# Kernel tuning notes

Hardware: AMD Instinct MI355X
Metric: run time of the kernel (lower is better)

Reference implementation:

```python
import jax, jax.numpy as jnp
import numpy as np

OUT_SIZE = 7
SAMPLE_NUM = 2
FINEST_SCALE = 56.0
STRIDES = (4, 8, 16, 32)
IMG_H, IMG_W = 800.0, 1216.0


def roi_align(feat, rois, out_size, spatial_scale, sr):
    """Vectorized RoIAlign (aligned=False / mmdet legacy semantics).
    feat: [B,C,H,W]; rois: [K,5] (batch_idx, x1, y1, x2, y2). Returns [K,C,out,out]."""
    B, C, H, W = feat.shape
    K = rois.shape[0]
    ft = jnp.transpose(feat, (0, 2, 3, 1))  # [B,H,W,C] for channel-last gathers
    b = rois[:, 0].astype(jnp.int32)
    x1 = rois[:, 1] * spatial_scale
    y1 = rois[:, 2] * spatial_scale
    x2 = rois[:, 3] * spatial_scale
    y2 = rois[:, 4] * spatial_scale
    roi_w = jnp.maximum(x2 - x1, 1.0)
    roi_h = jnp.maximum(y2 - y1, 1.0)
    bin_w = roi_w / out_size
    bin_h = roi_h / out_size
    G = out_size * sr  # sample grid points per spatial dim
    g = (jnp.arange(G, dtype=feat.dtype) + 0.5) / sr  # sub-bin centers in bin units
    ys = y1[:, None] + g[None, :] * bin_h[:, None]  # [K,G]
    xs = x1[:, None] + g[None, :] * bin_w[:, None]  # [K,G]
    # validity (points outside [-1, H]/[-1, W] contribute 0)
    vy = (ys >= -1.0) & (ys <= H)
    vx = (xs >= -1.0) & (xs <= W)
    valid = vy[:, :, None] & vx[:, None, :]  # [K,G,G]
    # clamp into the map, then bilinear interpolate
    ysc = jnp.clip(ys, 0.0, H - 1)
    xsc = jnp.clip(xs, 0.0, W - 1)
    y0 = jnp.floor(ysc)
    x0 = jnp.floor(xsc)
    ly = ysc - y0
    lx = xsc - x0
    y0i = y0.astype(jnp.int32)
    x0i = x0.astype(jnp.int32)

    def gather(yi, xi):  # yi:[K,G], xi:[K,G] -> [K,G,G,C]
        yc = jnp.clip(yi, 0, H - 1)
        xc = jnp.clip(xi, 0, W - 1)
        return ft[b[:, None, None], yc[:, :, None], xc[:, None, :], :]

    wy0 = (1.0 - ly)[:, :, None, None]
    wy1 = ly[:, :, None, None]
    wx0 = (1.0 - lx)[:, None, :, None]
    wx1 = lx[:, None, :, None]
    val = (gather(y0i, x0i) * (wy0 * wx0)
           + gather(y0i, x0i + 1) * (wy0 * wx1)
           + gather(y0i + 1, x0i) * (wy1 * wx0)
           + gather(y0i + 1, x0i + 1) * (wy1 * wx1))  # [K,G,G,C]
    val = val * valid[..., None]
    # average the sr x sr samples in each output bin
    val = val.reshape(K, out_size, sr, out_size, sr, C).mean(axis=(2, 4))
    return jnp.transpose(val, (0, 3, 1, 2))  # [K,C,out,out]


def map_roi_levels(rois, num_levels):
    scale = jnp.sqrt((rois[:, 3] - rois[:, 1] + 1.0) * (rois[:, 4] - rois[:, 2] + 1.0))
    lvl = jnp.floor(jnp.log2(scale / FINEST_SCALE + 1e-6))
    return jnp.clip(lvl, 0, num_levels - 1).astype(jnp.int32)


def setup_inputs() -> dict:
    key = jax.random.key(0)
    ks = jax.random.split(key, 10)
    feat0 = jax.random.normal(ks[0], (2, 256, 200, 304), dtype=jnp.float32)
    feat1 = jax.random.normal(ks[1], (2, 256, 100, 152), dtype=jnp.float32)
    feat2 = jax.random.normal(ks[2], (2, 256, 50, 76), dtype=jnp.float32)
    feat3 = jax.random.normal(ks[3], (2, 256, 25, 38), dtype=jnp.float32)
    K = 1024
    b = jax.random.randint(ks[4], (K,), 0, 2).astype(jnp.float32)
    # log-uniform box sizes in [16, 600] px so all 4 FPN levels are used
    logw = jax.random.uniform(ks[5], (K,), minval=np.log(16.0), maxval=np.log(600.0))
    logh = jax.random.uniform(ks[6], (K,), minval=np.log(16.0), maxval=np.log(600.0))
    w = jnp.exp(logw)
    h = jnp.exp(logh)
    cx = jax.random.uniform(ks[7], (K,), minval=0.0, maxval=IMG_W)
    cy = jax.random.uniform(ks[8], (K,), minval=0.0, maxval=IMG_H)
    x1 = jnp.clip(cx - w / 2, 0.0, IMG_W - 2.0)
    y1 = jnp.clip(cy - h / 2, 0.0, IMG_H - 2.0)
    x2 = jnp.clip(cx + w / 2, x1 + 1.0, IMG_W - 1.0)
    y2 = jnp.clip(cy + h / 2, y1 + 1.0, IMG_H - 1.0)
    rois = jnp.stack([b, x1, y1, x2, y2], axis=1).astype(jnp.float32)
    return {"feat0": feat0, "feat1": feat1, "feat2": feat2, "feat3": feat3, "rois": rois}


def reference(feat0, feat1, feat2, feat3, rois):
    feats = [feat0, feat1, feat2, feat3]
    num_levels = len(feats)
    lvls = map_roi_levels(rois, num_levels)  # [K]
    K = rois.shape[0]
    C = feats[0].shape[1]
    out = jnp.zeros((K, C, OUT_SIZE, OUT_SIZE), dtype=feats[0].dtype)
    for i in range(num_levels):
        pooled = roi_align(feats[i], rois, OUT_SIZE, 1.0 / STRIDES[i], SAMPLE_NUM)
        out = out + jnp.where((lvls == i)[:, None, None, None], pooled, 0.0)
    return out
```

## Files before the change

### kernel.cpp

```cpp
#include <hip/hip_runtime.h>
#include <math.h>


#define OUT_SZ 7
#define NCH 256
#define NBINS 49
#define NGROUPS 4

__global__ __launch_bounds__(256, 6)
void roi_align_direct(const float* __restrict__ f0, const float* __restrict__ f1,
                      const float* __restrict__ f2, const float* __restrict__ f3,
                      const float* __restrict__ rois,
                      float* __restrict__ out)
{
    const int k = blockIdx.x;
    const int g = blockIdx.y;
    const int t = threadIdx.x;
    const int w    = t >> 6;
    const int lane = t & 63;

    float rb   = rois[k * 5 + 0];
    float rix1 = rois[k * 5 + 1];
    float riy1 = rois[k * 5 + 2];
    float rix2 = rois[k * 5 + 3];
    float riy2 = rois[k * 5 + 4];

    float scale = sqrtf((rix2 - rix1 + 1.0f) * (riy2 - riy1 + 1.0f));
    int lvl = (int)floorf(log2f(scale * (1.0f / 56.0f) + 1e-6f));
    lvl = lvl < 0 ? 0 : (lvl > 3 ? 3 : lvl);

    float ss = 1.0f / (float)(4 << lvl);
    float x1 = rix1 * ss, y1 = riy1 * ss;
    float rw = fmaxf(rix2 * ss - x1, 1.0f);
    float rh = fmaxf(riy2 * ss - y1, 1.0f);
    float bw = rw * (1.0f / OUT_SZ);
    float bh = rh * (1.0f / OUT_SZ);
    const int H = 800  >> (2 + lvl);
    const int W = 1216 >> (2 + lvl);
    const float fH = (float)H, fW = (float)W;
    const float* fb = (lvl == 0) ? f0 : (lvl == 1) ? f1 : (lvl == 2) ? f2 : f3;
    const int HW = H * W;

    if (lane >= NBINS) return;
    const int bin = lane;
    const int oy = bin / OUT_SZ;
    const int ox = bin - oy * OUT_SZ;

    float lx[2], fvx[2]; int cx[2];
#pragma unroll
    for (int j = 0; j < 2; ++j) {
        float xs = x1 + ((float)(2 * ox + j) + 0.5f) * 0.5f * bw;
        fvx[j] = (xs >= -1.0f && xs <= fW) ? 1.0f : 0.0f;
        float xc = fminf(fmaxf(xs, 0.0f), fW - 1.0f);
        int x0 = (int)floorf(xc);
        x0 = min(x0, W - 2);
        lx[j] = xc - (float)x0;
        cx[j] = x0;
    }
    float ly[2], fvy[2]; int ry[2];
#pragma unroll
    for (int i = 0; i < 2; ++i) {
        float ysv = y1 + ((float)(2 * oy + i) + 0.5f) * 0.5f * bh;
        fvy[i] = (ysv >= -1.0f && ysv <= fH) ? 1.0f : 0.0f;
        float yc = fminf(fmaxf(ysv, 0.0f), fH - 1.0f);
        int y0 = (int)floorf(yc);
        y0 = min(y0, H - 2);
        ly[i] = yc - (float)y0;
        ry[i] = y0;
    }
    float wv00 = fvy[0] * fvx[0], wv01 = fvy[0] * fvx[1];
    float wv10 = fvy[1] * fvx[0], wv11 = fvy[1] * fvx[1];

    int off[8];
#pragma unroll
    for (int r = 0; r < 4; ++r) {
        int row = ry[r >> 1] + (r & 1);
        off[2 * r + 0] = row * W + cx[0];
        off[2 * r + 1] = row * W + cx[1];
    }

    const int ch0 = g * 64 + w;
    const float* chp = fb + (size_t)((int)rb * NCH + ch0) * HW;
    float* outp = out + ((size_t)k * NCH + ch0) * NBINS + bin;

#pragma unroll 2
    for (int i = 0; i < 16; ++i) {
        float v0[8], v1[8];
#pragma unroll
        for (int q = 0; q < 8; ++q) {
            v0[q] = chp[off[q]];
            v1[q] = chp[off[q] + 1];
        }
        float h[8];
#pragma unroll
        for (int q = 0; q < 8; ++q)
            h[q] = fmaf(lx[q & 1], v1[q] - v0[q], v0[q]);

        float s00 = fmaf(ly[0], h[2] - h[0], h[0]);
        float s01 = fmaf(ly[0], h[3] - h[1], h[1]);
        float s10 = fmaf(ly[1], h[6] - h[4], h[4]);
        float s11 = fmaf(ly[1], h[7] - h[5], h[5]);

        float acc = wv00 * s00 + wv01 * s01 + wv10 * s10 + wv11 * s11;
        *outp = acc * 0.25f;

        chp  += 4 * (size_t)HW;
        outp += 4 * NBINS;
    }
}

extern "C" void kernel_launch(void* const* d_in, const int* in_sizes, int n_in,
                              void* d_out, int out_size, void* d_ws, size_t ws_size,
                              hipStream_t stream)
{
    const float* f0   = (const float*)d_in[0];
    const float* f1   = (const float*)d_in[1];
    const float* f2   = (const float*)d_in[2];
    const float* f3   = (const float*)d_in[3];
    const float* rois = (const float*)d_in[4];
    float* out = (float*)d_out;

    int K = in_sizes[4] / 5;
    if (K <= 0) return;

    roi_align_direct<<<dim3(K, NGROUPS), 256, 0, stream>>>(f0, f1, f2, f3, rois, out);
}
```

Baseline: 304.8 us.

## Gather bilinear taps with aligned vector loads and precomputed separable weights

Replaces the eight pairs of scalar loads per channel with aligned float4 (or float2 when W is not a multiple of 4) loads covering both x-samples. Rows and columns shared between the two sub-samples are merged into per-lane weights, and loads for rows whose weight is zero are skipped. This aims to cut the number of memory instructions in a gather-bound kernel. In exchange it adds weight setup work, predicated loads and possible register pressure, and it drops the unroll-2 on the channel loop.

```diff
diff --git a/kernel.cpp b/kernel.cpp
--- a/kernel.cpp
+++ b/kernel.cpp
@@ -7,11 +7,127 @@
 #define NBINS 49
 #define NGROUPS 4
 
+template<int A>
+__device__ __forceinline__ void roi_gather(
+    const float* __restrict__ chp, float* __restrict__ outp,
+    int W, int H, size_t chstep,
+    float x1, float y1, float bw, float bh, int oy, int ox)
+{
+    const float fH = (float)H, fW = (float)W;
+
+    float lxv[2], fxv[2]; int cxv[2];
+#pragma unroll
+    for (int j = 0; j < 2; ++j) {
+        float xs = x1 + ((float)(2 * ox + j) + 0.5f) * 0.5f * bw;
+        fxv[j] = (xs >= -1.0f && xs <= fW) ? 1.0f : 0.0f;
+        float xc = fminf(fmaxf(xs, 0.0f), fW - 1.0f);
+        int x0 = (int)floorf(xc);
+        x0 = min(x0, W - 2);
+        lxv[j] = xc - (float)x0;
+        cxv[j] = x0;
+    }
+    float lyv[2], fyv[2]; int ryv[2];
+#pragma unroll
+    for (int i = 0; i < 2; ++i) {
+        float ys = y1 + ((float)(2 * oy + i) + 0.5f) * 0.5f * bh;
+        fyv[i] = (ys >= -1.0f && ys <= fH) ? 1.0f : 0.0f;
+        float yc = fminf(fmaxf(ys, 0.0f), fH - 1.0f);
+        int y0 = (int)floorf(yc);
+        y0 = min(y0, H - 2);
+        lyv[i] = yc - (float)y0;
+        ryv[i] = y0;
+    }
+
+    const int i00 = cxv[0] & (A - 1), i01 = cxv[1] & (A - 1);
+    const int a0  = cxv[0] - i00,     a1  = cxv[1] - i01;
+    const bool sq  = (a1 == a0);
+    const bool of0 = (i00 == A - 1);
+    const bool of1 = (i01 == A - 1);
+    const float c00 = fxv[0] * (1.0f - lxv[0]), c01 = fxv[0] * lxv[0];
+    const float c10 = fxv[1] * (1.0f - lxv[1]), c11 = fxv[1] * lxv[1];
+
+    float wA[A], wB[A];
+#pragma unroll
+    for (int m = 0; m < A; ++m) {
+        float v = 0.0f;
+        v += (i00 == m) ? c00 : 0.0f;
+        v += (!of0 && (i00 + 1 == m)) ? c01 : 0.0f;
+        v += (sq && (i01 == m)) ? c10 : 0.0f;
+        v += (sq && !of1 && (i01 + 1 == m)) ? c11 : 0.0f;
+        wA[m] = v;
+        wB[m] = (!sq) ? (((i01 == m) ? c10 : 0.0f) +
+                         ((!of1 && (i01 + 1 == m)) ? c11 : 0.0f))
+                      : 0.0f;
+    }
+    const float wf0 = (of0 ? c01 : 0.0f) + ((sq && of1) ? c11 : 0.0f);
+    const float wf1 = (!sq && of1) ? c11 : 0.0f;
+    const bool useB  = !sq;
+    const bool useF0 = of0 || (sq && of1);
+    const bool useF1 = !sq && of1;
+
+    const int dy = ryv[1] - ryv[0];
+    const float wy0 = fyv[0] * (1.0f - lyv[0]) +
+                      ((dy == 0) ? fyv[1] * (1.0f - lyv[1]) : 0.0f);
+    const float wy1 = fyv[0] * lyv[0] +
+                      ((dy == 0) ? fyv[1] * lyv[1]
+                                 : ((dy == 1) ? fyv[1] * (1.0f - lyv[1]) : 0.0f));
+    const float wy2 = (dy >= 2) ? fyv[1] * (1.0f - lyv[1]) : 0.0f;
+    const float wy3 = (dy >= 1) ? fyv[1] * lyv[1] : 0.0f;
+
+    const float wys[4] = {wy0, wy1, wy2, wy3};
+    int offA[4], offB[4];
+    {
+        const int rows0 = ryv[0], rows1 = ryv[0] + 1;
+        const int rows2 = ryv[1], rows3 = ryv[1] + 1;
+        offA[0] = rows0 * W + a0;  offB[0] = rows0 * W + a1;
+        offA[1] = rows1 * W + a0;  offB[1] = rows1 * W + a1;
+        offA[2] = rows2 * W + a0;  offB[2] = rows2 * W + a1;
+        offA[3] = rows3 * W + a0;  offB[3] = rows3 * W + a1;
+    }
+
+    const float* p = chp;
+    float* o = outp;
+    for (int c = 0; c < 16; ++c) {
+        float acc = 0.0f;
+#pragma unroll
+        for (int r = 0; r < 4; ++r) {
+            const float wy = wys[r];
+            const bool rv = (wy != 0.0f);
+            float qa[A], qb[A];
+            if (A == 4) {
+                float4 va = rv ? *(const float4*)(p + offA[r])
+                               : make_float4(0.f, 0.f, 0.f, 0.f);
+                qa[0] = va.x; qa[1] = va.y; qa[2] = va.z; qa[3] = va.w;
+                float4 vb = (rv && useB) ? *(const float4*)(p + offB[r])
+                                         : make_float4(0.f, 0.f, 0.f, 0.f);
+                qb[0] = vb.x; qb[1] = vb.y; qb[2] = vb.z; qb[3] = vb.w;
+            } else {
+                float2 va = rv ? *(const float2*)(p + offA[r])
+                               : make_float2(0.f, 0.f);
+                qa[0] = va.x; qa[1] = va.y;
+                float2 vb = (rv && useB) ? *(const float2*)(p + offB[r])
+                                         : make_float2(0.f, 0.f);
+                qb[0] = vb.x; qb[1] = vb.y;
+            }
+            float f0 = (rv && useF0) ? p[offA[r] + A] : 0.0f;
+            float f1 = (rv && useF1) ? p[offB[r] + A] : 0.0f;
+            float h = f0 * wf0 + f1 * wf1;
+#pragma unroll
+            for (int m = 0; m < A; ++m)
+                h += qa[m] * wA[m] + qb[m] * wB[m];
+            acc += wy * h;
+        }
+        *o = acc * 0.25f;
+        p += chstep;
+        o += 4 * NBINS;
+    }
+}
+
 __global__ __launch_bounds__(256, 6)
-void roi_align_direct(const float* __restrict__ f0, const float* __restrict__ f1,
-                      const float* __restrict__ f2, const float* __restrict__ f3,
-                      const float* __restrict__ rois,
-                      float* __restrict__ out)
+void roi_align_sep(const float* __restrict__ f0, const float* __restrict__ f1,
+                   const float* __restrict__ f2, const float* __restrict__ f3,
+                   const float* __restrict__ rois,
+                   float* __restrict__ out)
 {
     const int k = blockIdx.x;
     const int g = blockIdx.y;
@@ -37,7 +153,7 @@
     float bh = rh * (1.0f / OUT_SZ);
     const int H = 800  >> (2 + lvl);
     const int W = 1216 >> (2 + lvl);
-    const float fH = (float)H, fW = (float)W;
+
     const float* fb = (lvl == 0) ? f0 : (lvl == 1) ? f1 : (lvl == 2) ? f2 : f3;
     const int HW = H * W;
 
@@ -46,66 +162,14 @@
     const int oy = bin / OUT_SZ;
     const int ox = bin - oy * OUT_SZ;
 
-    float lx[2], fvx[2]; int cx[2];
-#pragma unroll
-    for (int j = 0; j < 2; ++j) {
-        float xs = x1 + ((float)(2 * ox + j) + 0.5f) * 0.5f * bw;
-        fvx[j] = (xs >= -1.0f && xs <= fW) ? 1.0f : 0.0f;
-        float xc = fminf(fmaxf(xs, 0.0f), fW - 1.0f);
-        int x0 = (int)floorf(xc);
-        x0 = min(x0, W - 2);
-        lx[j] = xc - (float)x0;
-        cx[j] = x0;
-    }
-    float ly[2], fvy[2]; int ry[2];
-#pragma unroll
-    for (int i = 0; i < 2; ++i) {
-        float ysv = y1 + ((float)(2 * oy + i) + 0.5f) * 0.5f * bh;
-        fvy[i] = (ysv >= -1.0f && ysv <= fH) ? 1.0f : 0.0f;
-        float yc = fminf(fmaxf(ysv, 0.0f), fH - 1.0f);
-        int y0 = (int)floorf(yc);
-        y0 = min(y0, H - 2);
-        ly[i] = yc - (float)y0;
-        ry[i] = y0;
-    }
-    float wv00 = fvy[0] * fvx[0], wv01 = fvy[0] * fvx[1];
-    float wv10 = fvy[1] * fvx[0], wv11 = fvy[1] * fvx[1];
-
-    int off[8];
-#pragma unroll
-    for (int r = 0; r < 4; ++r) {
-        int row = ry[r >> 1] + (r & 1);
-        off[2 * r + 0] = row * W + cx[0];
-        off[2 * r + 1] = row * W + cx[1];
-    }
-
     const int ch0 = g * 64 + w;
     const float* chp = fb + (size_t)((int)rb * NCH + ch0) * HW;
     float* outp = out + ((size_t)k * NCH + ch0) * NBINS + bin;
 
-#pragma unroll 2
-    for (int i = 0; i < 16; ++i) {
-        float v0[8], v1[8];
-#pragma unroll
-        for (int q = 0; q < 8; ++q) {
-            v0[q] = chp[off[q]];
-            v1[q] = chp[off[q] + 1];
-        }
-        float h[8];
-#pragma unroll
-        for (int q = 0; q < 8; ++q)
-            h[q] = fmaf(lx[q & 1], v1[q] - v0[q], v0[q]);
-
-        float s00 = fmaf(ly[0], h[2] - h[0], h[0]);
-        float s01 = fmaf(ly[0], h[3] - h[1], h[1]);
-        float s10 = fmaf(ly[1], h[6] - h[4], h[4]);
-        float s11 = fmaf(ly[1], h[7] - h[5], h[5]);
-
-        float acc = wv00 * s00 + wv01 * s01 + wv10 * s10 + wv11 * s11;
-        *outp = acc * 0.25f;
-
-        chp  += 4 * (size_t)HW;
-        outp += 4 * NBINS;
+    if (W & 3) {
+        roi_gather<2>(chp, outp, W, H, 4 * (size_t)HW, x1, y1, bw, bh, oy, ox);
+    } else {
+        roi_gather<4>(chp, outp, W, H, 4 * (size_t)HW, x1, y1, bw, bh, oy, ox);
     }
 }
 
@@ -123,5 +187,5 @@
     int K = in_sizes[4] / 5;
     if (K <= 0) return;
 
-    roi_align_direct<<<dim3(K, NGROUPS), 256, 0, stream>>>(f0, f1, f2, f3, rois, out);
+    roi_align_sep<<<dim3(K, NGROUPS), 256, 0, stream>>>(f0, f1, f2, f3, rois, out);
 }
```

Measured after the change: 320.2 us. +5.0%, slower.

## Sort ROIs by image, level and Morton code, then map blocks to XCDs

Applied to the files above, without the earlier changes.

Adds a single-block bitonic sort kernel that orders ROIs by batch image, FPN level and a Morton code of their center. The main kernel then remaps blockIdx so that each XCD (blocks are taken round-robin mod 8) processes a contiguous range of spatially nearby ROIs. The aim is better L2 reuse of feature-map reads on the chiplet design. The cost is an extra serial sort launch on one block, plus an indirection load per block.

```diff
diff --git a/kernel.cpp b/kernel.cpp
--- a/kernel.cpp
+++ b/kernel.cpp
@@ -6,14 +6,77 @@
 #define NCH 256
 #define NBINS 49
 #define NGROUPS 4
+#define SORT_N 2048
+
+__global__ __launch_bounds__(256, 8)
+void roi_sort_kernel(const float* __restrict__ rois, int K, int N,
+                     int* __restrict__ perm)
+{
+    __shared__ unsigned long long s[SORT_N];
+    const int t = threadIdx.x;
+
+    for (int i = t; i < N; i += 256) {
+        unsigned key = 0xFFFFFFFFu;
+        if (i < K) {
+            float rb = rois[i * 5 + 0];
+            float x1 = rois[i * 5 + 1], y1 = rois[i * 5 + 2];
+            float x2 = rois[i * 5 + 3], y2 = rois[i * 5 + 4];
+            float scale = sqrtf((x2 - x1 + 1.0f) * (y2 - y1 + 1.0f));
+            int lvl = (int)floorf(log2f(scale * (1.0f / 56.0f) + 1e-6f));
+            lvl = lvl < 0 ? 0 : (lvl > 3 ? 3 : lvl);
+            float ss = 1.0f / (float)(4 << lvl);
+            float Wf = 1216.0f * ss, Hf = 800.0f * ss;
+            float cx = 0.5f * (x1 + x2) * ss;
+            float cy = 0.5f * (y1 + y2) * ss;
+            float qxf = cx * (128.0f / Wf);
+            float qyf = cy * (128.0f / Hf);
+            int qx = (int)fminf(fmaxf(qxf, 0.0f), 127.0f);
+            int qy = (int)fminf(fmaxf(qyf, 0.0f), 127.0f);
+            unsigned m = 0;
+#pragma unroll
+            for (int bb = 0; bb < 7; ++bb)
+                m |= (((unsigned)(qx >> bb) & 1u) << (2 * bb)) |
+                     (((unsigned)(qy >> bb) & 1u) << (2 * bb + 1));
+            unsigned img = (rb > 0.5f) ? 1u : 0u;
+            key = (((img * 4u + (unsigned)lvl) << 14) | m);
+        }
+        s[i] = ((unsigned long long)key << 32) | (unsigned)i;
+    }
+    __syncthreads();
+
+    for (int size = 2; size <= N; size <<= 1) {
+        for (int stride = size >> 1; stride > 0; stride >>= 1) {
+            for (int tid = t; tid < N / 2; tid += 256) {
+                int lo = tid & (stride - 1);
+                int i = ((tid - lo) << 1) + lo;
+                int j = i + stride;
+                bool asc = ((i & size) == 0);
+                unsigned long long a = s[i], b = s[j];
+                if ((a > b) == asc) { s[i] = b; s[j] = a; }
+            }
+            __syncthreads();
+        }
+    }
+
+    for (int i = t; i < K; i += 256)
+        perm[i] = (int)(unsigned)(s[i] & 0xFFFFFFFFu);
+}
 
 __global__ __launch_bounds__(256, 6)
 void roi_align_direct(const float* __restrict__ f0, const float* __restrict__ f1,
                       const float* __restrict__ f2, const float* __restrict__ f3,
                       const float* __restrict__ rois,
+                      const int* __restrict__ perm, int K,
                       float* __restrict__ out)
 {
-    const int k = blockIdx.x;
+    int k;
+    {
+        const int orig = blockIdx.x;
+        const int q = K >> 3, r = K & 7;
+        const int xcd = orig & 7, pos = orig >> 3;
+        int idx = (xcd < r ? xcd * (q + 1) : r * (q + 1) + (xcd - r) * q) + pos;
+        k = perm ? perm[idx] : idx;
+    }
     const int g = blockIdx.y;
     const int t = threadIdx.x;
     const int w    = t >> 6;
@@ -123,5 +186,14 @@
     int K = in_sizes[4] / 5;
     if (K <= 0) return;
 
-    roi_align_direct<<<dim3(K, NGROUPS), 256, 0, stream>>>(f0, f1, f2, f3, rois, out);
+    int* perm = nullptr;
+    if (K <= SORT_N && d_ws && ws_size >= (size_t)K * sizeof(int)) {
+        perm = (int*)d_ws;
+        int N = 1;
+        while (N < K) N <<= 1;
+        roi_sort_kernel<<<1, 256, 0, stream>>>(rois, K, N, perm);
+    }
+
+    roi_align_direct<<<dim3(K, NGROUPS), 256, 0, stream>>>(
+        f0, f1, f2, f3, rois, perm, K, out);
 }
```

Result: slower. 319.6 us (+4.9%).
